# Kernel optimization log

Hardware: AMD Instinct MI355X
Metric: run time of the kernel (lower is better)

The kernel has to match this reference:

```python
import jax, jax.numpy as jnp
import numpy as np
from jax import lax

Tx, Ty, NA, NS = 30, 10, 32, 64
HV, MV = 128, 64
B = 16384


def setup_inputs() -> dict:
    key = jax.random.key(0)
    ks = jax.random.split(key, 16)
    g = lambda k, s: jax.random.normal(k, s, jnp.float32) * 0.05
    return {
        "X": jax.random.normal(ks[0], (B, Tx, HV), jnp.float32),
        # pre-attention bidirectional LSTM (PyTorch gate order i,f,g,o; b = b_ih + b_hh)
        "W_ih_f": g(ks[1], (4 * NA, HV)), "W_hh_f": g(ks[2], (4 * NA, NA)), "b_f": g(ks[3], (4 * NA,)),
        "W_ih_r": g(ks[4], (4 * NA, HV)), "W_hh_r": g(ks[5], (4 * NA, NA)), "b_r": g(ks[6], (4 * NA,)),
        # attention MLP
        "W1": g(ks[7], (10, 2 * NA + NS)), "b1": g(ks[8], (10,)),
        "W2": g(ks[9], (1, 10)), "b2": g(ks[10], (1,)),
        # post-attention LSTM cell
        "W_ih_p": g(ks[11], (4 * NS, 2 * NA)), "W_hh_p": g(ks[12], (4 * NS, NS)), "b_p": g(ks[13], (4 * NS,)),
        # output projection
        "Wo": g(ks[14], (MV, NS)), "bo": g(ks[15], (MV,)),
    }


def _cell(x, h, c, W_ih, W_hh, b):
    # PyTorch LSTM cell, gate order (i, f, g, o)
    z = x @ W_ih.T + h @ W_hh.T + b
    i, f, gg, o = jnp.split(z, 4, axis=-1)
    c = jax.nn.sigmoid(f) * c + jax.nn.sigmoid(i) * jnp.tanh(gg)
    h = jax.nn.sigmoid(o) * jnp.tanh(c)
    return h, c


def _run_lstm(X, W_ih, W_hh, b):
    Bn = X.shape[0]
    H = W_hh.shape[1]
    init = (jnp.zeros((Bn, H), X.dtype), jnp.zeros((Bn, H), X.dtype))

    def step(carry, x_t):
        h, c = _cell(x_t, carry[0], carry[1], W_ih, W_hh, b)
        return (h, c), h

    _, hs = lax.scan(step, init, jnp.swapaxes(X, 0, 1))  # hs: [Tx, B, H]
    return jnp.swapaxes(hs, 0, 1)


def reference(X, W_ih_f, W_hh_f, b_f, W_ih_r, W_hh_r, b_r, W1, b1, W2, b2,
              W_ih_p, W_hh_p, b_p, Wo, bo):
    # bidirectional encoder: a is [B, Tx, 2*NA]
    a_f = _run_lstm(X, W_ih_f, W_hh_f, b_f)
    a_r = _run_lstm(X[:, ::-1, :], W_ih_r, W_hh_r, b_r)[:, ::-1, :]
    a = jnp.concatenate([a_f, a_r], axis=-1)
    Bn = X.shape[0]

    def dec_step(carry, _):
        s, c = carry
        # one_step_attention
        s_rep = jnp.broadcast_to(s[:, None, :], (Bn, Tx, NS))
        cat = jnp.concatenate([a, s_rep], axis=-1)          # [B, Tx, 2*NA+NS]
        e = jnp.tanh(cat @ W1.T + b1)                        # [B, Tx, 10]
        en = jax.nn.relu(e @ W2.T + b2)                      # [B, Tx, 1]
        alphas = jax.nn.softmax(en, axis=1)                  # softmax over Tx
        context = jnp.sum(alphas * a, axis=1)                # [B, 2*NA]
        # post-attention LSTM (single step)
        s, c = _cell(context, s, c, W_ih_p, W_hh_p, b_p)
        out = s @ Wo.T + bo                                  # [B, MV]
        return (s, c), out

    init = (jnp.zeros((Bn, NS), X.dtype), jnp.zeros((Bn, NS), X.dtype))
    _, outs = lax.scan(dec_step, init, None, length=Ty)      # [Ty, B, MV]
    return jnp.swapaxes(outs, 0, 1)                          # [B, Ty, MV]
```

## Files before the change

kernel.cpp:

```cpp
#include <hip/hip_runtime.h>

typedef unsigned short u16;
typedef unsigned int   u32;
typedef __attribute__((ext_vector_type(8))) short short8;
typedef __attribute__((ext_vector_type(4))) float f4;

#define BT 8
#define TX 30
#define TY 10

__device__ __forceinline__ float bf2f_u16(u16 h){ u32 i=((u32)h)<<16; float f; __builtin_memcpy(&f,&i,4); return f; }
__device__ __forceinline__ float lo2f(u32 p){ u32 i=p<<16; float f; __builtin_memcpy(&f,&i,4); return f; }
__device__ __forceinline__ float hi2f(u32 p){ u32 i=p&0xffff0000u; float f; __builtin_memcpy(&f,&i,4); return f; }
__device__ __forceinline__ u16 f2bf(float f){ u32 x; __builtin_memcpy(&x,&f,4); u32 r=(x+0x7fffu+((x>>16)&1u))>>16; return (u16)r; }

#if __has_builtin(__builtin_amdgcn_rcpf)
__device__ __forceinline__ float frcp(float x){ return __builtin_amdgcn_rcpf(x); }
#else
__device__ __forceinline__ float frcp(float x){ return 1.0f/x; }
#endif
__device__ __forceinline__ float sigm(float x){ return frcp(1.0f+__expf(-x)); }
__device__ __forceinline__ float tanh_(float x){ x=fminf(fmaxf(x,-15.0f),15.0f); float e=__expf(2.0f*x); return 1.0f - 2.0f*frcp(e+1.0f); }

__device__ __forceinline__ f4 mfma16(short8 a, short8 b, f4 c){
    return __builtin_amdgcn_mfma_f32_16x16x32_bf16(a, b, c, 0, 0, 0);
}

union S8u { short8 s; u32 u[4]; };

__device__ __forceinline__ void cvt_pair(float a0, float a1, u32& hp, u32& lp){
    u32 u0, u1; __builtin_memcpy(&u0,&a0,4); __builtin_memcpy(&u1,&a1,4);
    hp = __builtin_amdgcn_perm(u1, u0, 0x07060302u);
    float r0 = a0 - hi2f(u0);
    float r1 = a1 - hi2f(u1);
    u32 v0, v1; __builtin_memcpy(&v0,&r0,4); __builtin_memcpy(&v1,&r1,4);
    lp = __builtin_amdgcn_perm(v1, v0, 0x07060302u);
}

struct SDec {
    float aW1[BT][TX][10];
    u16 sh[BT][72], sl[BT][72];
    u16 ctxh[BT][72], ctxl[BT][72];
    u16 zr2[72];
    float sW1[BT][12];
    float en[BT][32];
    float w2b[12]; float b2s;
};
struct SEnc {
    u16 h[2][2][2][BT][40];
    u16 zr[40];
};
union UU { SEnc e; SDec d; };
struct Smem {
    u16 a[BT][TX][72];
    UU u;
};

__global__ __launch_bounds__(256, 3) void fused_kernel(
    const float* __restrict__ X,
    const float* __restrict__ Wihf, const float* __restrict__ Whhf, const float* __restrict__ bfv,
    const float* __restrict__ Wihr, const float* __restrict__ Whhr, const float* __restrict__ brv,
    const float* __restrict__ W1, const float* __restrict__ b1, const float* __restrict__ W2, const float* __restrict__ b2,
    const float* __restrict__ Wihp, const float* __restrict__ Whhp, const float* __restrict__ bp,
    const float* __restrict__ Wo, const float* __restrict__ bo,
    float* __restrict__ out)
{
    __shared__ __align__(16) Smem sm;
    const int tid = threadIdx.x;
    const int b0  = blockIdx.x * BT;

    {
        u32* p = (u32*)&sm.u.e;
        for (int i = tid; i < (int)(sizeof(SEnc)/4); i += 256) p[i] = 0u;
    }
    __syncthreads();

    const int lane = tid & 63;
    const int wv   = tid >> 6;
    const int mL   = lane & 15;
    const int qL   = lane >> 4;
    const int k0q  = qL * 8;
    const int ed   = wv >> 1;
    const int ub   = (wv & 1) * 16;
    const int sstep= mL >> 3;

    const float* Wih = ed ? Wihr : Wihf;
    const float* Whh = ed ? Whhr : Whhf;
    const float* bv  = ed ? brv  : bfv;

    short8 Bih[4][4]; short8 Bhh[4]; float bias4[4];
    #pragma unroll
    for (int gt = 0; gt < 4; gt++){
        const int n = gt*32 + ub + mL;
        #pragma unroll
        for (int kt = 0; kt < 4; kt++){
            const float* p = Wih + n*128 + kt*32 + k0q;
            short8 s;
            #pragma unroll
            for (int j = 0; j < 8; j++) s[j] = (short)f2bf(p[j]);
            Bih[gt][kt] = s;
        }
        {
            const float* p = Whh + n*32 + k0q;
            short8 s;
            #pragma unroll
            for (int j = 0; j < 8; j++) s[j] = (short)f2bf(p[j]);
            Bhh[gt] = s;
        }
        bias4[gt] = bv[n];
    }

    const float* xrow = X + ((long)(b0 + (mL & 7))) * TX * 128;
    float cst[4] = {0.f,0.f,0.f,0.f};

    auto epair = [&](int t, f4* cur, f4* nxt){
        if (t + 2 < TX){
            const int ts = ed ? (TX-1-(t+2+sstep)) : (t+2+sstep);
            const float* p = xrow + ts*128 + k0q;
            #pragma unroll
            for (int kt = 0; kt < 4; kt++){
                nxt[2*kt]   = *(const f4*)(p + kt*32);
                nxt[2*kt+1] = *(const f4*)(p + kt*32 + 4);
            }
        }
        const int rb = (t+1) & 1, wb = t & 1;

        f4 acc[4];
        #pragma unroll
        for (int gt = 0; gt < 4; gt++) acc[gt] = (f4){bias4[gt],bias4[gt],bias4[gt],bias4[gt]};

        #pragma unroll
        for (int kt = 0; kt < 4; kt++){
            S8u xh, xl;
            #pragma unroll
            for (int pp = 0; pp < 4; pp++){
                const f4 v = cur[2*kt + (pp>>1)];
                const int e = (pp & 1) * 2;
                cvt_pair(v[e], v[e+1], xh.u[pp], xl.u[pp]);
            }
            #pragma unroll
            for (int gt = 0; gt < 4; gt++){
                acc[gt] = mfma16(xh.s, Bih[gt][kt], acc[gt]);
                acc[gt] = mfma16(xl.s, Bih[gt][kt], acc[gt]);
            }
        }
        {
            const short8 Ahh = *(const short8*)((mL < 8) ? &sm.u.e.h[rb][ed][0][mL][k0q] : &sm.u.e.zr[k0q]);
            const short8 Ahl = *(const short8*)((mL < 8) ? &sm.u.e.h[rb][ed][1][mL][k0q] : &sm.u.e.zr[k0q]);
            #pragma unroll
            for (int gt = 0; gt < 4; gt++){
                acc[gt] = mfma16(Ahh, Bhh[gt], acc[gt]);
                acc[gt] = mfma16(Ahl, Bhh[gt], acc[gt]);
            }
        }
        if (qL < 2){
            const int tpos = ed ? (TX-1-t) : t;
            #pragma unroll
            for (int reg = 0; reg < 4; reg++){
                const int m = qL*4 + reg;
                const float ii = sigm(acc[0][reg]), ff = sigm(acc[1][reg]);
                const float gg = tanh_(acc[2][reg]), oo = sigm(acc[3][reg]);
                cst[reg] = ff*cst[reg] + ii*gg;
                const float hh = oo * tanh_(cst[reg]);
                const u16 hhi = f2bf(hh);
                const u16 hlo = f2bf(hh - bf2f_u16(hhi));
                sm.u.e.h[wb][ed][0][m][ub+mL] = hhi;
                sm.u.e.h[wb][ed][1][m][ub+mL] = hlo;
                sm.a[m][tpos][ed*32 + ub + mL] = hhi;
            }
        }
        #pragma unroll
        for (int reg = 0; reg < 4; reg++) cst[reg] = __shfl_xor(cst[reg], 32);
        __syncthreads();
        {
            const short8 Ahh = *(const short8*)((mL >= 8) ? &sm.u.e.h[wb][ed][0][mL-8][k0q] : &sm.u.e.zr[k0q]);
            const short8 Ahl = *(const short8*)((mL >= 8) ? &sm.u.e.h[wb][ed][1][mL-8][k0q] : &sm.u.e.zr[k0q]);
            #pragma unroll
            for (int gt = 0; gt < 4; gt++){
                acc[gt] = mfma16(Ahh, Bhh[gt], acc[gt]);
                acc[gt] = mfma16(Ahl, Bhh[gt], acc[gt]);
            }
        }
        if (qL >= 2){
            const int tpos = ed ? (TX-2-t) : (t+1);
            #pragma unroll
            for (int reg = 0; reg < 4; reg++){
                const int m = (qL-2)*4 + reg;
                const float ii = sigm(acc[0][reg]), ff = sigm(acc[1][reg]);
                const float gg = tanh_(acc[2][reg]), oo = sigm(acc[3][reg]);
                cst[reg] = ff*cst[reg] + ii*gg;
                const float hh = oo * tanh_(cst[reg]);
                const u16 hhi = f2bf(hh);
                const u16 hlo = f2bf(hh - bf2f_u16(hhi));
                sm.u.e.h[rb][ed][0][m][ub+mL] = hhi;
                sm.u.e.h[rb][ed][1][m][ub+mL] = hlo;
                sm.a[m][tpos][ed*32 + ub + mL] = hhi;
            }
        }
        #pragma unroll
        for (int reg = 0; reg < 4; reg++) cst[reg] = __shfl_xor(cst[reg], 32);
        __syncthreads();
    };

    f4 rawA[8], rawB[8];
    {
        const int ts0 = ed ? (TX-1-sstep) : sstep;
        const float* p = xrow + ts0*128 + k0q;
        #pragma unroll
        for (int kt = 0; kt < 4; kt++){
            rawA[2*kt]   = *(const f4*)(p + kt*32);
            rawA[2*kt+1] = *(const f4*)(p + kt*32 + 4);
        }
    }
    for (int tp = 0; tp < 28; tp += 4){ epair(tp, rawA, rawB); epair(tp+2, rawB, rawA); }
    epair(28, rawA, rawB);

    {
        u32* z = (u32*)sm.u.d.sh;
        for (int i = tid; i < (4*BT*72 + 72)/2; i += 256) z[i] = 0u;
    }
    if (tid < 10) sm.u.d.w2b[tid] = W2[tid];
    if (tid == 0) sm.u.d.b2s = b2[0];

    short8 W1aB[2][2];
    #pragma unroll
    for (int kt = 0; kt < 2; kt++){
        short8 hv8, lv8;
        #pragma unroll
        for (int j = 0; j < 8; j++){
            const float v = (mL < 10) ? W1[mL*128 + kt*32 + k0q + j] : 0.f;
            const u16 hb = f2bf(v);
            hv8[j] = (short)hb;
            lv8[j] = (short)f2bf(v - bf2f_u16(hb));
        }
        W1aB[kt][0] = hv8; W1aB[kt][1] = lv8;
    }
    const float b1v = (mL < 10) ? b1[mL] : 0.f;

    for (int tile = wv; tile < 15; tile += 4){
        f4 accA = (f4){b1v, b1v, b1v, b1v};
        const u16* abase = &sm.a[0][0][0] + (tile*16 + mL)*72;
        #pragma unroll
        for (int kt = 0; kt < 2; kt++){
            const short8 av = *(const short8*)(abase + kt*32 + k0q);
            accA = mfma16(av, W1aB[kt][0], accA);
            accA = mfma16(av, W1aB[kt][1], accA);
        }
        if (mL < 10){
            #pragma unroll
            for (int reg = 0; reg < 4; reg++){
                const int r = tile*16 + qL*4 + reg;
                (&sm.u.d.aW1[0][0][0])[r*10 + mL] = accA[reg];
            }
        }
    }

    const int uw = wv * 16;
    short8 Bip[4][2], Bhp[4][2]; float pb4[4];
    #pragma unroll
    for (int gt = 0; gt < 4; gt++){
        const int n = gt*64 + uw + mL;
        #pragma unroll
        for (int kt = 0; kt < 2; kt++){
            const float* p = Wihp + n*64 + kt*32 + k0q;
            const float* q = Whhp + n*64 + kt*32 + k0q;
            short8 s1v, s2v;
            #pragma unroll
            for (int j = 0; j < 8; j++){ s1v[j] = (short)f2bf(p[j]); s2v[j] = (short)f2bf(q[j]); }
            Bip[gt][kt] = s1v; Bhp[gt][kt] = s2v;
        }
        pb4[gt] = bp[n];
    }
    short8 Bo2[2];
    {
        const int n = uw + mL;
        #pragma unroll
        for (int kt = 0; kt < 2; kt++){
            const float* p = Wo + n*64 + kt*32 + k0q;
            short8 s;
            #pragma unroll
            for (int j = 0; j < 8; j++) s[j] = (short)f2bf(p[j]);
            Bo2[kt] = s;
        }
    }
    short8 W1sB[2];
    #pragma unroll
    for (int kt = 0; kt < 2; kt++){
        short8 s;
        #pragma unroll
        for (int j = 0; j < 8; j++){
            const float v = (mL < 10) ? W1[mL*128 + 64 + kt*32 + k0q + j] : 0.f;
            s[j] = (short)f2bf(v);
        }
        W1sB[kt] = s;
    }
    const float boL = bo[uw + mL];
    float cs2[4] = {0.f,0.f,0.f,0.f};
    __syncthreads();

    for (int ty = 0; ty < TY; ty++){
        {
            f4 accW = (f4){0.f,0.f,0.f,0.f};
            #pragma unroll
            for (int kt = 0; kt < 2; kt++){
                const int ko = kt*32 + k0q;
                const short8 shh = *(const short8*)((mL < 8) ? &sm.u.d.sh[mL][ko] : &sm.u.d.zr2[ko]);
                const short8 sll = *(const short8*)((mL < 8) ? &sm.u.d.sl[mL][ko] : &sm.u.d.zr2[ko]);
                accW = mfma16(shh, W1sB[kt], accW);
                accW = mfma16(sll, W1sB[kt], accW);
            }
            if (qL < 2 && mL < 10 && wv == 0){
                #pragma unroll
                for (int reg = 0; reg < 4; reg++) sm.u.d.sW1[qL*4+reg][mL] = accW[reg];
            }
        }
        __syncthreads();
        if (tid < 240){
            const int er = tid/30, et = tid - er*30;
            float env = sm.u.d.b2s;
            #pragma unroll
            for (int j = 0; j < 10; j++){
                const float z = sm.u.d.aW1[er][et][j] + sm.u.d.sW1[er][j];
                env += sm.u.d.w2b[j]*tanh_(z);
            }
            sm.u.d.en[er][et] = fmaxf(env, 0.f);
        }
        __syncthreads();
        {
            const int cr = tid >> 5, cup = tid & 31;
            const float* enr = sm.u.d.en[cr];
            float mx = enr[0];
            #pragma unroll
            for (int t2 = 1; t2 < TX; t2++) mx = fmaxf(mx, enr[t2]);
            float ssum = 0.f, s0 = 0.f, s1 = 0.f;
            const u16* ap = &sm.a[cr][0][2*cup];
            #pragma unroll 5
            for (int t2 = 0; t2 < TX; t2++){
                const float e = __expf(enr[t2]-mx);
                const u32 pa = *(const u32*)(ap + t2*72);
                ssum += e;
                s0 += e*lo2f(pa); s1 += e*hi2f(pa);
            }
            const float inv = frcp(ssum);
            s0 *= inv; s1 *= inv;
            const u16 h0 = f2bf(s0), h1 = f2bf(s1);
            const u16 l0 = f2bf(s0 - bf2f_u16(h0)), l1 = f2bf(s1 - bf2f_u16(h1));
            *(u32*)&sm.u.d.ctxh[cr][2*cup] = (u32)h0 | ((u32)h1 << 16);
            *(u32*)&sm.u.d.ctxl[cr][2*cup] = (u32)l0 | ((u32)l1 << 16);
        }
        __syncthreads();
        f4 acc2[4];
        #pragma unroll
        for (int gt = 0; gt < 4; gt++) acc2[gt] = (f4){pb4[gt],pb4[gt],pb4[gt],pb4[gt]};
        #pragma unroll
        for (int kt = 0; kt < 2; kt++){
            const int ko = kt*32 + k0q;
            const bool v8 = (mL < 8);
            const short8 ch  = *(const short8*)(v8 ? &sm.u.d.ctxh[mL][ko] : &sm.u.d.zr2[ko]);
            const short8 cl  = *(const short8*)(v8 ? &sm.u.d.ctxl[mL][ko] : &sm.u.d.zr2[ko]);
            const short8 shh = *(const short8*)(v8 ? &sm.u.d.sh[mL][ko]   : &sm.u.d.zr2[ko]);
            const short8 sll = *(const short8*)(v8 ? &sm.u.d.sl[mL][ko]   : &sm.u.d.zr2[ko]);
            #pragma unroll
            for (int gt = 0; gt < 4; gt++){
                acc2[gt] = mfma16(ch,  Bip[gt][kt], acc2[gt]);
                acc2[gt] = mfma16(cl,  Bip[gt][kt], acc2[gt]);
                acc2[gt] = mfma16(shh, Bhp[gt][kt], acc2[gt]);
                acc2[gt] = mfma16(sll, Bhp[gt][kt], acc2[gt]);
            }
        }
        __syncthreads();
        if (qL < 2){
            #pragma unroll
            for (int reg = 0; reg < 4; reg++){
                const int m = qL*4 + reg;
                const float ii = sigm(acc2[0][reg]), ff = sigm(acc2[1][reg]);
                const float gg = tanh_(acc2[2][reg]), oo = sigm(acc2[3][reg]);
                cs2[reg] = ff*cs2[reg] + ii*gg;
                const float sv = oo * tanh_(cs2[reg]);
                const u16 shi = f2bf(sv);
                const u16 slo = f2bf(sv - bf2f_u16(shi));
                sm.u.d.sh[m][uw+mL]  = shi;
                sm.u.d.sl[m][uw+mL]  = slo;
            }
        }
        __syncthreads();
        f4 acc3 = (f4){boL, boL, boL, boL};
        #pragma unroll
        for (int kt = 0; kt < 2; kt++){
            const int ko = kt*32 + k0q;
            const short8 shh = *(const short8*)((mL < 8) ? &sm.u.d.sh[mL][ko] : &sm.u.d.zr2[ko]);
            const short8 sll = *(const short8*)((mL < 8) ? &sm.u.d.sl[mL][ko] : &sm.u.d.zr2[ko]);
            acc3 = mfma16(shh, Bo2[kt], acc3);
            acc3 = mfma16(sll, Bo2[kt], acc3);
        }
        if (qL < 2){
            #pragma unroll
            for (int reg = 0; reg < 4; reg++){
                const int m = qL*4 + reg;
                out[(((long)(b0+m))*TY + ty)*64 + uw + mL] = acc3[reg];
            }
        }
    }
}

extern "C" void kernel_launch(void* const* d_in, const int* in_sizes, int n_in,
                              void* d_out, int out_size, void* d_ws, size_t ws_size,
                              hipStream_t stream) {
    const float* X    = (const float*)d_in[0];
    const float* Wihf = (const float*)d_in[1];
    const float* Whhf = (const float*)d_in[2];
    const float* bfv  = (const float*)d_in[3];
    const float* Wihr = (const float*)d_in[4];
    const float* Whhr = (const float*)d_in[5];
    const float* brv  = (const float*)d_in[6];
    const float* W1   = (const float*)d_in[7];
    const float* b1   = (const float*)d_in[8];
    const float* W2   = (const float*)d_in[9];
    const float* b2   = (const float*)d_in[10];
    const float* Wihp = (const float*)d_in[11];
    const float* Whhp = (const float*)d_in[12];
    const float* bp   = (const float*)d_in[13];
    const float* Wo   = (const float*)d_in[14];
    const float* bo   = (const float*)d_in[15];
    float* out = (float*)d_out;

    const int B = in_sizes[0] / (TX * 128);
    dim3 grid(B / BT), block(256);
    hipLaunchKernelGGL(fused_kernel, grid, block, 0, stream,
                       X, Wihf, Whhf, bfv, Wihr, Whhr, brv,
                       W1, b1, W2, b2, Wihp, Whhp, bp, Wo, bo, out);
}
```

Before: 752.9 us.

## Stage encoder inputs into LDS via async global_load_lds with swizzled layout

Replaces per-thread register double-buffering of X rows with asynchronous global-to-LDS loads (global_load_lds) into a double-buffered, XOR-swizzled shared-memory staging area, issued two timesteps ahead. Each wave then reads its MFMA A-operands from LDS. This frees the 16 f4 registers the old prefetch buffers held and removes the register cost of the prefetch, at the cost of more LDS (which may reduce blocks per CU) and reliance on the per-step barrier for visibility. The padded row stride of the attention buffer 'a' is also shrunk from 72 to 64, saving LDS but possibly adding bank conflicts.

Result: slower. 798.8 us (+6.1%).

```diff
diff --git a/kernel.cpp b/kernel.cpp
--- a/kernel.cpp
+++ b/kernel.cpp
@@ -24,6 +24,11 @@
 
 __device__ __forceinline__ f4 mfma16(short8 a, short8 b, f4 c){
     return __builtin_amdgcn_mfma_f32_16x16x32_bf16(a, b, c, 0, 0, 0);
+}
+
+__device__ __forceinline__ void gload_lds16(const float* g, float* l){
+    __builtin_amdgcn_global_load_lds((const __attribute__((address_space(1))) void*)g,
+                                     (__attribute__((address_space(3))) void*)l, 16, 0, 0);
 }
 
 union S8u { short8 s; u32 u[4]; };
@@ -49,10 +54,11 @@
 struct SEnc {
     u16 h[2][2][2][BT][40];
     u16 zr[40];
+    float xs[2][2][2][BT][128];
 };
 union UU { SEnc e; SDec d; };
 struct Smem {
-    u16 a[BT][TX][72];
+    u16 a[BT][TX][64];
     UU u;
 };
 
@@ -69,12 +75,6 @@
     const int tid = threadIdx.x;
     const int b0  = blockIdx.x * BT;
 
-    {
-        u32* p = (u32*)&sm.u.e;
-        for (int i = tid; i < (int)(sizeof(SEnc)/4); i += 256) p[i] = 0u;
-    }
-    __syncthreads();
-
     const int lane = tid & 63;
     const int wv   = tid >> 6;
     const int mL   = lane & 15;
@@ -82,7 +82,32 @@
     const int k0q  = qL * 8;
     const int ed   = wv >> 1;
     const int ub   = (wv & 1) * 16;
+    const int row8 = mL & 7;
     const int sstep= mL >> 3;
+
+    auto stage = [&](int t){
+        if (t >= TX) return;
+        float* xb = &sm.u.e.xs[(t>>1)&1][ed][0][0][0];
+        const int cbase = (wv & 1) * 4;
+        #pragma unroll
+        for (int c = 0; c < 4; c++){
+            const int P   = (cbase + c)*64 + lane;
+            const int st  = P >> 8;
+            const int rw  = (P >> 5) & 7;
+            const int pkb = P & 31;
+            const int kb  = (pkb & 24) | ((pkb & 7) ^ rw);
+            const int ts  = ed ? (TX-1-(t+st)) : (t+st);
+            const float* src = X + ((long)(b0 + rw))*TX*128 + ts*128 + kb*4;
+            gload_lds16(src, xb + (cbase + c)*256);
+        }
+    };
+
+    {
+        u32* p = (u32*)&sm.u.e;
+        for (int i = tid; i < 1300; i += 256) p[i] = 0u;
+    }
+    stage(0);
+    __syncthreads();
 
     const float* Wih = ed ? Wihr : Wihf;
     const float* Whh = ed ? Whhr : Whhf;
@@ -110,34 +135,30 @@
         bias4[gt] = bv[n];
     }
 
-    const float* xrow = X + ((long)(b0 + (mL & 7))) * TX * 128;
     float cst[4] = {0.f,0.f,0.f,0.f};
 
-    auto epair = [&](int t, f4* cur, f4* nxt){
-        if (t + 2 < TX){
-            const int ts = ed ? (TX-1-(t+2+sstep)) : (t+2+sstep);
-            const float* p = xrow + ts*128 + k0q;
-            #pragma unroll
-            for (int kt = 0; kt < 4; kt++){
-                nxt[2*kt]   = *(const f4*)(p + kt*32);
-                nxt[2*kt+1] = *(const f4*)(p + kt*32 + 4);
-            }
-        }
+    auto epair = [&](int t){
+        stage(t + 2);
         const int rb = (t+1) & 1, wb = t & 1;
 
+        const float* xb = &sm.u.e.xs[(t>>1)&1][ed][0][0][0];
+        const int rbase = (sstep*8 + row8)*32;
+
         f4 acc[4];
         #pragma unroll
         for (int gt = 0; gt < 4; gt++) acc[gt] = (f4){bias4[gt],bias4[gt],bias4[gt],bias4[gt]};
 
         #pragma unroll
         for (int kt = 0; kt < 4; kt++){
+            const int pA = kt*8 + ((qL*2)     ^ row8);
+            const int pB = kt*8 + ((qL*2 + 1) ^ row8);
+            const f4 v0 = *(const f4*)(xb + (rbase + pA)*4);
+            const f4 v1 = *(const f4*)(xb + (rbase + pB)*4);
             S8u xh, xl;
-            #pragma unroll
-            for (int pp = 0; pp < 4; pp++){
-                const f4 v = cur[2*kt + (pp>>1)];
-                const int e = (pp & 1) * 2;
-                cvt_pair(v[e], v[e+1], xh.u[pp], xl.u[pp]);
-            }
+            cvt_pair(v0[0], v0[1], xh.u[0], xl.u[0]);
+            cvt_pair(v0[2], v0[3], xh.u[1], xl.u[1]);
+            cvt_pair(v1[0], v1[1], xh.u[2], xl.u[2]);
+            cvt_pair(v1[2], v1[3], xh.u[3], xl.u[3]);
             #pragma unroll
             for (int gt = 0; gt < 4; gt++){
                 acc[gt] = mfma16(xh.s, Bih[gt][kt], acc[gt]);
@@ -202,18 +223,7 @@
         __syncthreads();
     };
 
-    f4 rawA[8], rawB[8];
-    {
-        const int ts0 = ed ? (TX-1-sstep) : sstep;
-        const float* p = xrow + ts0*128 + k0q;
-        #pragma unroll
-        for (int kt = 0; kt < 4; kt++){
-            rawA[2*kt]   = *(const f4*)(p + kt*32);
-            rawA[2*kt+1] = *(const f4*)(p + kt*32 + 4);
-        }
-    }
-    for (int tp = 0; tp < 28; tp += 4){ epair(tp, rawA, rawB); epair(tp+2, rawB, rawA); }
-    epair(28, rawA, rawB);
+    for (int tp = 0; tp < TX; tp += 2) epair(tp);
 
     {
         u32* z = (u32*)sm.u.d.sh;
@@ -239,7 +249,7 @@
 
     for (int tile = wv; tile < 15; tile += 4){
         f4 accA = (f4){b1v, b1v, b1v, b1v};
-        const u16* abase = &sm.a[0][0][0] + (tile*16 + mL)*72;
+        const u16* abase = &sm.a[0][0][0] + (tile*16 + mL)*64;
         #pragma unroll
         for (int kt = 0; kt < 2; kt++){
             const short8 av = *(const short8*)(abase + kt*32 + k0q);
@@ -337,7 +347,7 @@
             #pragma unroll 5
             for (int t2 = 0; t2 < TX; t2++){
                 const float e = __expf(enr[t2]-mx);
-                const u32 pa = *(const u32*)(ap + t2*72);
+                const u32 pa = *(const u32*)(ap + t2*64);
                 ssum += e;
                 s0 += e*lo2f(pa); s1 += e*hi2f(pa);
             }
```
